# Kernel optimization log

Hardware: AMD Instinct MI355X
Metric: run time of the kernel (lower is better)

Reference implementation:

```python
import jax, jax.numpy as jnp
import numpy as np

N_ITER, N_TAPS, N_DELAY, N_SRC = 2, 4, 1, 4
EPS = 1e-3
TINY = 1e-20
BATCH, N_CHAN, N_FREQ, N_FRAMES = 2, 6, 320, 500


def mag_sq(x):
    return x.real ** 2 + x.imag ** 2


def divide(num, denom, eps):
    return num / jnp.maximum(denom, eps)


def make_xbar(X, n_taps, n_delay):
    # X: (..., c, f, n) -> X_bar: (..., c, f, t, n); tap t is X delayed by n_delay + t
    n = X.shape[-1]
    pad = [(0, 0)] * (X.ndim - 1)
    taps = [jnp.pad(X, pad + [(n_delay + t, 0)])[..., :n] for t in range(n_taps)]
    return jnp.stack(taps, axis=-2)


def background_update(W, H, C_XX, C_XbarX, eps=1e-5):
    # recompute J from W, H and input covariances (ridge-loaded solve)
    n_src = W.shape[-3]
    A1 = jnp.einsum('...sfc,...cfd->...fsd', W, C_XX)
    A2 = jnp.einsum('...sfdt,...dtfc->...fsc', H, C_XbarX)
    Am = A1 + A2
    mat = Am[..., :n_src]
    load = jnp.abs(jnp.diagonal(mat, axis1=-2, axis2=-1)).sum(axis=-1)[..., None, None]
    load = jnp.maximum(load * eps, eps) * jnp.eye(n_src, dtype=mat.dtype)
    load = jax.lax.stop_gradient(load)
    J_H = jnp.linalg.solve(mat + load, Am[..., n_src:])
    return jnp.moveaxis(J_H.conj(), -1, -3)  # (..., n_bak, f, n_src)


def iss_type1(src, Y, w, eps):
    n = Y.shape[-1]
    Ys = Y[..., src, :, :]
    vn = jnp.einsum('...cfn,...cfn,...fn->...cf', w, Y, Ys.conj()) / n
    vd = jnp.einsum('...cfn,...fn->...cf', w, mag_sq(Ys)) / n
    v = divide(vn, vd, eps)
    vs = 1.0 - 1.0 / jnp.sqrt(jnp.maximum(vd[..., src, :], eps))
    return v.at[..., src, :].set(vs.astype(v.dtype))


def iss_type2(Y, Zs, w, eps):
    vn = jnp.einsum('...cfn,...cfn,...fn->...cf', w, Y, Zs.conj())
    vd = jnp.einsum('...cfn,...fn->...cf', w, mag_sq(Zs))
    return divide(vn, vd, eps)


def iss_type3(src, tap, Y, X_bar, w, eps):
    Xst = X_bar[..., src, :, tap, :]
    vn = jnp.einsum('...cfn,...cfn,...fn->...cf', w, Y, Xst.conj())
    vd = jnp.einsum('...cfn,...fn->...cf', w, mag_sq(Xst))
    return divide(vn, vd, eps)


def mat_up1(W, H, A, v, src, eps):
    Wn = W - jnp.einsum('...cf,...fd->...cfd', v, W[..., src, :, :])
    Hn = H - jnp.einsum('...cf,...fdt->...cfdt', v, H[..., src, :, :, :])
    u = jnp.einsum('...sfc,...cf->...sf', A[..., :v.shape[-2]], v)
    u = u / (1.0 - v[..., src:src + 1, :] + eps)
    return Wn, Hn, A.at[..., src].add(u)


def mat_up2(W, J, A, v, g, eps):
    n_src = W.shape[-3]
    v2 = v[..., :n_src, :] + jnp.einsum('...sfc,...cf->...sf', W[..., n_src:], v[..., n_src:, :])
    W1 = W[..., :n_src] - jnp.einsum('...cf,...fd->...cfd', v[..., :n_src, :], g)
    Wn = jnp.concatenate([W1, W[..., n_src:]], axis=-1)
    Jn = J - jnp.einsum('...cf,...fd->...cfd', v[..., n_src:, :], g)
    Av = jnp.einsum('...sfc,...cf->...sf', A[..., :v2.shape[-2]], v2)
    gA = jnp.einsum('...fs,...sfc->...fc', g, A[..., :g.shape[-1], :, :])
    denom = 1.0 - jnp.einsum('...cf,...fc->...f', v2, gA)
    mul = denom.conj() / (mag_sq(denom) + eps)
    An = A + jnp.einsum('...sf,...fc->...sfc', Av, gA * mul[..., None])
    return Wn, Jn, An


def bak_update_vector(p, d, g, eps):
    gdg = jnp.sum(mag_sq(g) / (d + eps), axis=-2)
    gdp = jnp.sum(g.conj() * p / (d + eps), axis=-2)
    b = 1.0 - gdp
    b1 = mag_sq(b)
    a = b1 * gdg + TINY
    beta = (-b1 + jnp.sqrt(b1 ** 2 + 4.0 * a)) / (2.0 * a)
    ell1 = beta * b
    ell2 = (1.0 / jnp.sqrt(eps + gdg)).astype(ell1.dtype)
    ell = jnp.where(b1 > eps ** 2, ell1, ell2)
    return (p - ell[..., None, :] * g) / (d + eps)


def bak_update(bak, Y, Z, X, W, J, A, w, eps):
    n_src, n_freq, n_frames = Y.shape[-3:]
    n_chan = X.shape[-3]
    Zs = Z[..., bak, :, :] + X[..., n_src + bak, :, :]
    norm = 1.0 / n_frames
    ones = jnp.ones(w.shape[:-3] + (n_chan - n_src, n_freq, n_frames), w.dtype)
    wz = jnp.concatenate([w, ones], axis=-3)
    YZ = jnp.concatenate([Y, Z], axis=-3)
    p = jnp.einsum('...cfn,...cfn,...fn->...cf', YZ, wz, Zs.conj()) * norm
    d = jnp.einsum('...cfn,...fn->...cf', wz, mag_sq(Zs)) * norm
    A2 = jnp.concatenate([A, jnp.einsum('...sfc,...cfd->...sfd', A, W[..., n_src:])], axis=-1)
    g = jnp.einsum('...fs,...sfc->...cf', J[..., bak, :, :], A2).conj()
    v = bak_update_vector(p, d, g, eps)
    YZ = YZ - jnp.einsum('...cf,...fn->...cfn', v, Zs)
    return v, YZ[..., :n_src, :, :], YZ[..., n_src:, :, :]


def iss_updates(Y, X, X_bar, W, H, A, w, J, Z, eps):
    n_src = Y.shape[-3]
    n_chan = X.shape[-3]
    n_taps = X_bar.shape[-2]
    n_bak = n_chan - n_src
    # 1) background rows (structured type-2 updates)
    for bak in range(n_bak):
        v, Y, Z = bak_update(bak, Y, Z, X, W, J, A, w, eps)
        g = J[..., bak, :, :]
        W, J, A = mat_up2(W, J, A, v, g, eps)
    # 2) source directions (type 1)
    for src in range(n_src):
        v = iss_type1(src, Y, w, eps)
        Y = Y - jnp.einsum('...cf,...fn->...cfn', v, Y[..., src, :, :])
        W, H, A = mat_up1(W, H, A, v, src, eps)
    # 3) background directions (type 2)
    for bak in range(n_bak):
        v = iss_type2(Y, Z[..., bak, :, :], w, eps)
        Y = Y - jnp.einsum('...cf,...fn->...cfn', v, Z[..., bak, :, :])
        W = W.at[..., :n_src].add(-jnp.einsum('...cf,...fd->...cfd', v, J[..., bak, :, :]))
        W = W.at[..., n_src + bak].add(v)
    if n_bak > 0:
        # keep A consistent: A = inv(W1 + W2 J) per frequency
        Binv = W[..., :n_src] + jnp.einsum('...sfc,...cfd->...sfd', W[..., n_src:], J)
        A = jnp.moveaxis(jnp.linalg.inv(jnp.moveaxis(Binv, -2, -3)), -3, -2)
    # 4) dereverberation taps (type 3)
    for src in range(n_chan):
        for tap in range(n_taps):
            v = iss_type3(src, tap, Y, X_bar, w, eps)
            Y = Y - jnp.einsum('...cf,...fn->...cfn', v, X_bar[..., src, :, tap, :])
            H = H.at[..., src, tap].add(v)
    return Y, Z, W, H, J, A


def _forward(X):
    batch = X.shape[:-3]
    n_chan, n_freq, n_frames = X.shape[-3:]
    n_src = N_SRC
    X_bar = make_xbar(X, N_TAPS, N_DELAY)
    W = jnp.broadcast_to(jnp.eye(n_src, n_chan, dtype=X.dtype)[:, None, :], batch + (n_src, n_freq, n_chan))
    H = jnp.zeros(batch + (n_src, n_freq, n_chan, N_TAPS), X.dtype)
    A = jnp.broadcast_to(jnp.eye(n_src, dtype=X.dtype)[:, None, :], batch + (n_src, n_freq, n_src))
    # initialize background demixing J from input second-order statistics
    C_XX = jnp.einsum('...cfn,...dfn->...cfd', X, X.conj()) / n_frames
    C_XbarX = jnp.einsum('...dftn,...cfn->...dtfc', X_bar, X.conj()) / n_frames
    J = background_update(W, H, C_XX, C_XbarX)
    Y = X[..., :n_src, :, :]
    Z = jnp.einsum('...cfd,...dfn->...cfn', J, X[..., :n_src, :, :]) - X[..., n_src:, :, :]
    for _ in range(N_ITER):
        # Gauss (time-varying) source-model weights, shared across frequencies
        w = 1.0 / jnp.maximum(jnp.mean(mag_sq(Y), axis=-2, keepdims=True), EPS)
        w = jnp.broadcast_to(w, Y.shape)
        Y, Z, W, H, J, A = iss_updates(Y, X, X_bar, W, H, A, w, J, Z, EPS)
    return Y


def setup_inputs():
    key = jax.random.key(0)
    k1, k2 = jax.random.split(key)
    shape = (BATCH, N_CHAN, N_FREQ, N_FRAMES)
    return {"X_real": jax.random.normal(k1, shape, jnp.float32),
            "X_imag": jax.random.normal(k2, shape, jnp.float32)}


def reference(X_real, X_imag):
    X = jax.lax.complex(X_real, X_imag)
    return _forward(X)
```

## Files before the change

kernel.cpp:

```cpp
#include <hip/hip_runtime.h>

#define NFR 500
#define NFQ 320
#define NB  2
#define NC  6
#define NS  4
#define NBK 2
#define NT  4
#define NDLY 1
#define EPSF 1e-3f
#define TINYF 1e-20f

#define NP   512
#define XPAD 8
#define XLEN (XPAD + NP)
#define NCH  8
#define FPC  (NFQ / NCH)

typedef float f2 __attribute__((ext_vector_type(2)));

__device__ __forceinline__ f2 mk2(float r, float i){ f2 t; t.x = r; t.y = i; return t; }
__device__ __forceinline__ f2 cmul(f2 a, f2 b){ return a.xx*b + a.yy*mk2(-b.y, b.x); }
__device__ __forceinline__ f2 cmulc(f2 a, f2 b){ return b.xx*a + b.yy*mk2(a.y, -a.x); }
__device__ __forceinline__ f2 conjc(f2 a){ return mk2(a.x, -a.y); }
__device__ __forceinline__ float cmag2(f2 a){ return a.x*a.x + a.y*a.y; }
__device__ __forceinline__ f2 cinv(f2 a){ float m = a.x*a.x + a.y*a.y; return mk2(a.x/m, -a.y/m); }

#define DPPF(x, ctrl) __int_as_float(__builtin_amdgcn_mov_dpp(__float_as_int(x), (ctrl), 0xF, 0xF, true))
__device__ __forceinline__ float wred64(float x){
  x += DPPF(x, 0x111);
  x += DPPF(x, 0x112);
  x += DPPF(x, 0x114);
  x += DPPF(x, 0x118);
  x += DPPF(x, 0x142);
  x += DPPF(x, 0x143);
  return __int_as_float(__builtin_amdgcn_readlane(__float_as_int(x), 63));
}

__global__ __launch_bounds__(256) void k_init(
  const float* __restrict__ Xr, const float* __restrict__ Xi,
  f2* __restrict__ Yg, f2* __restrict__ Zg,
  f2* __restrict__ Wg, f2* __restrict__ Jg, f2* __restrict__ Ag)
{
  __shared__ f2 sX[NC][NFR];
  __shared__ f2 sC[NS][NC];
  __shared__ f2 sJl[NBK][NS];

  const int bf = blockIdx.x;
  const int b = bf / NFQ, f = bf % NFQ;
  const int tid = threadIdx.x, wv = tid >> 6, lane = tid & 63;

  for (int c = 0; c < NC; ++c) {
    const size_t base = ((size_t)(b*NC + c)*NFQ + f)*NFR;
    for (int n = tid; n < NFR; n += 256)
      sX[c][n] = mk2(Xr[base+n], Xi[base+n]);
  }
  __syncthreads();

  for (int p = wv; p < NS*NC; p += 4) {
    int s = p / NC, d = p % NC;
    f2 ar2 = mk2(0.f,0.f), ai2 = mk2(0.f,0.f);
    for (int n = lane; n < NFR; n += 64) {
      f2 xs = sX[s][n], xd = sX[d][n];
      ar2 += xs * xd;
      ai2 += xs.yx * mk2(xd.x, -xd.y);
    }
    float ar = wred64(ar2.x + ar2.y), ai = wred64(ai2.x + ai2.y);
    if (lane == 0) sC[s][d] = mk2(ar*(1.f/NFR), ai*(1.f/NFR));
  }
  __syncthreads();

  if (tid == 0) {
    f2 M[NS][NC];
    for (int s = 0; s < NS; ++s)
      for (int d = 0; d < NC; ++d) M[s][d] = sC[s][d];
    float dsum = 0.f;
    for (int s = 0; s < NS; ++s) dsum += sqrtf(cmag2(M[s][s]));
    float load = fmaxf(dsum*1e-5f, 1e-5f);
    for (int s = 0; s < NS; ++s) M[s][s].x += load;
    for (int col = 0; col < NS; ++col) {
      int piv = col; float best = cmag2(M[col][col]);
      for (int r = col+1; r < NS; ++r) { float m = cmag2(M[r][col]); if (m > best){best=m; piv=r;} }
      if (piv != col) for (int k = 0; k < NC; ++k) { f2 t=M[col][k]; M[col][k]=M[piv][k]; M[piv][k]=t; }
      f2 ip = cinv(M[col][col]);
      for (int k = col; k < NC; ++k) M[col][k] = cmul(M[col][k], ip);
      for (int r = 0; r < NS; ++r) if (r != col) {
        f2 fac = M[r][col];
        for (int k = col; k < NC; ++k) M[r][k] -= cmul(fac, M[col][k]);
      }
    }
    for (int k = 0; k < NBK; ++k)
      for (int s = 0; s < NS; ++s) sJl[k][s] = conjc(M[s][NS+k]);
  }
  __syncthreads();

  if (tid < NBK*NS) {
    int k = tid / NS, s = tid % NS;
    Jg[((size_t)(b*NBK+k)*NFQ + f)*NS + s] = sJl[k][s];
  } else if (tid < NBK*NS + NS*NC) {
    int t = tid - NBK*NS; int s = t / NC, d = t % NC;
    Wg[((size_t)(b*NS+s)*NFQ + f)*NC + d] = (s==d) ? mk2(1.f,0.f) : mk2(0.f,0.f);
  } else if (tid < NBK*NS + NS*NC + NS*NS) {
    int t = tid - NBK*NS - NS*NC; int s = t / NS, d = t % NS;
    Ag[((size_t)(b*NS+s)*NFQ + f)*NS + d] = (s==d) ? mk2(1.f,0.f) : mk2(0.f,0.f);
  }
  for (int c = 0; c < NS; ++c) {
    const size_t base = ((size_t)(b*NS + c)*NFQ + f)*NFR;
    for (int n = tid; n < NFR; n += 256) Yg[base+n] = sX[c][n];
  }
  for (int k = 0; k < NBK; ++k) {
    const size_t base = ((size_t)(b*NBK + k)*NFQ + f)*NFR;
    for (int n = tid; n < NFR; n += 256) {
      f2 acc = -sX[NS+k][n];
      for (int s = 0; s < NS; ++s) acc += cmul(sJl[k][s], sX[s][n]);
      Zg[base+n] = acc;
    }
  }
}

__global__ __launch_bounds__(512) void k_wpart(const f2* __restrict__ Yg,
                                               float* __restrict__ wacc)
{
  const int bs = blockIdx.x / NCH;
  const int ch = blockIdx.x % NCH;
  const int n  = threadIdx.x;
  if (n >= NFR) return;
  const f2* row = Yg + (size_t)bs*NFQ*NFR;
  f2 acc2 = mk2(0.f,0.f);
  for (int ff = 0; ff < FPC; ++ff) {
    f2 y = row[(size_t)(ch*FPC + ff)*NFR + n];
    acc2 += y*y;
  }
  wacc[((size_t)(ch*NB*NS + bs))*NFR + n] = acc2.x + acc2.y;
}

__global__ __launch_bounds__(256, 4) void k_iter(
  const float* __restrict__ Xr, const float* __restrict__ Xi,
  f2* __restrict__ Yg, f2* __restrict__ Zg,
  f2* __restrict__ Wg, f2* __restrict__ Jg, f2* __restrict__ Ag,
  const float* __restrict__ wacc, float* __restrict__ outR, const int last)
{
  __shared__ f2 sXp[NC][XLEN];
  __shared__ f2 sZ[NBK][NP];
  __shared__ f2 sS[NP];
  __shared__ f2 sW[NS][NC];
  __shared__ f2 sJ[NBK][NS];
  __shared__ f2 sA[NS][NS];
  __shared__ f2 sB[NS][2*NS];
  __shared__ f2 sv[NC], sg[NC], sgo[NS], sp[NC];
  __shared__ float sd[NC];
  __shared__ f2 sAv[NS], sgA[NS], sWsrc[NC];

  const int bf = blockIdx.x;
  const int b = bf / NFQ, f = bf % NFQ;
  const int tid = threadIdx.x, wv = tid >> 6, lane = tid & 63;

  f2 yreg[8];
  float wreg[8];

  for (int c = 0; c < NC; ++c) {
    const size_t base = ((size_t)(b*NC + c)*NFQ + f)*NFR;
    for (int j = tid; j < XLEN; j += 256) {
      int n = j - XPAD;
      sXp[c][j] = (n >= 0 && n < NFR) ? mk2(Xr[base+n], Xi[base+n]) : mk2(0.f,0.f);
    }
  }
  for (int k = 0; k < NBK; ++k) {
    const size_t zb = ((size_t)(b*NBK + k)*NFQ + f)*NFR;
    for (int n = tid; n < NP; n += 256) sZ[k][n] = (n < NFR) ? Zg[zb+n] : mk2(0.f,0.f);
  }
  {
    const size_t yb = ((size_t)(b*NS + wv)*NFQ + f)*NFR;
    const int bs = b*NS + wv;
#pragma unroll
    for (int i = 0; i < 8; ++i) {
      int n = lane + 64*i;
      if (n < NFR) {
        yreg[i] = Yg[yb+n];
        float a = 0.f;
#pragma unroll
        for (int ch = 0; ch < NCH; ++ch) a += wacc[((size_t)(ch*NB*NS + bs))*NFR + n];
        wreg[i] = 1.0f / fmaxf(a * (1.0f/(float)NFQ), EPSF);
      } else { yreg[i] = mk2(0.f,0.f); wreg[i] = 0.f; }
    }
  }
  if (tid < NS*NC) sW[tid/NC][tid%NC] = Wg[((size_t)(b*NS + tid/NC)*NFQ + f)*NC + tid%NC];
  else if (tid < NS*NC + NBK*NS) { int t=tid-NS*NC; sJ[t/NS][t%NS] = Jg[((size_t)(b*NBK+t/NS)*NFQ+f)*NS + t%NS]; }
  else if (tid < NS*NC + NBK*NS + NS*NS) { int t=tid-NS*NC-NBK*NS; sA[t/NS][t%NS] = Ag[((size_t)(b*NS+t/NS)*NFQ+f)*NS + t%NS]; }
  __syncthreads();

  f2 vloc[NC];

  for (int bak = 0; bak < NBK; ++bak) {
    for (int n = tid; n < NP; n += 256)
      sS[n] = sZ[bak][n] + sXp[NS+bak][XPAD+n];
    if (bak > 0 && tid < 16) {
      int s = tid >> 2, c = tid & 3;
      f2 v2[NS];
#pragma unroll
      for (int t = 0; t < NS; ++t)
        v2[t] = vloc[t] + cmul(sW[t][NS+0], vloc[NS+0]) + cmul(sW[t][NS+1], vloc[NS+1]);
      f2 den = mk2(1.f,0.f);
#pragma unroll
      for (int cc = 0; cc < NS; ++cc) den -= cmul(v2[cc], sgA[cc]);
      float m2 = cmag2(den) + EPSF;
      f2 mul = mk2(den.x/m2, -den.y/m2);
      sA[s][c] += cmul(sAv[s], cmul(sgA[c], mul));
    }
    __syncthreads();

    f2 zs[8];
    {
      f2 pr2 = mk2(0.f,0.f), pi2 = mk2(0.f,0.f), dd2 = mk2(0.f,0.f);
#pragma unroll
      for (int i = 0; i < 8; ++i) {
        zs[i] = sS[lane+64*i];
        f2 wy = wreg[i]*yreg[i];
        pr2 += wy * zs[i];
        pi2 += wy.yx * mk2(zs[i].x, -zs[i].y);
        dd2 += (wreg[i]*zs[i]) * zs[i];
      }
      float pr = wred64(pr2.x+pr2.y), pi = wred64(pi2.x+pi2.y), dd = wred64(dd2.x+dd2.y);
      if (lane == 0) { sp[wv] = mk2(pr*(1.f/NFR), pi*(1.f/NFR)); sd[wv] = dd*(1.f/NFR); }
      if (wv < NBK) {
        f2 qr2 = mk2(0.f,0.f), qi2 = mk2(0.f,0.f), qd2 = mk2(0.f,0.f);
#pragma unroll
        for (int i = 0; i < 8; ++i) {
          f2 y = sZ[wv][lane+64*i];
          qr2 += y * zs[i];
          qi2 += y.yx * mk2(zs[i].x, -zs[i].y);
          qd2 += zs[i]*zs[i];
        }
        float qr = wred64(qr2.x+qr2.y), qi = wred64(qi2.x+qi2.y), qd = wred64(qd2.x+qd2.y);
        if (lane == 0) { sp[NS+wv] = mk2(qr*(1.f/NFR), qi*(1.f/NFR)); sd[NS+wv] = qd*(1.f/NFR); }
      }
    }
    if (tid < NC) {
      int c = tid; f2 acc = mk2(0.f,0.f);
      for (int s = 0; s < NS; ++s) {
        f2 a2;
        if (c < NS) a2 = sA[s][c];
        else {
          a2 = mk2(0.f,0.f);
          for (int k = 0; k < NS; ++k) a2 += cmul(sA[s][k], sW[k][c]);
        }
        acc += cmul(sJ[bak][s], a2);
      }
      sg[c] = conjc(acc);
    } else if (tid >= 8 && tid < 8+NS) {
      sgo[tid-8] = sJ[bak][tid-8];
    }
    __syncthreads();

    {
      float gdg = 0.f; f2 gdp = mk2(0.f,0.f);
#pragma unroll
      for (int c = 0; c < NC; ++c) {
        f2 gc = sg[c]; float id = 1.0f/(sd[c] + EPSF);
        gdg += cmag2(gc) * id;
        gdp += id * cmulc(sp[c], gc);
      }
      f2 bb = mk2(1.0f - gdp.x, -gdp.y);
      float b1 = cmag2(bb);
      float a = b1*gdg + TINYF;
      float beta = (-b1 + sqrtf(b1*b1 + 4.0f*a)) / (2.0f*a);
      f2 ell = (b1 > EPSF*EPSF) ? (beta*bb) : mk2(1.0f/sqrtf(EPSF + gdg), 0.f);
#pragma unroll
      for (int c = 0; c < NC; ++c)
        vloc[c] = (1.0f/(sd[c] + EPSF)) * (sp[c] - cmul(ell, sg[c]));
    }
    {
      f2 vc = vloc[wv];
#pragma unroll
      for (int i = 0; i < 8; ++i) yreg[i] -= cmul(vc, zs[i]);
      if (wv < NBK) {
        f2 v2c = vloc[NS+wv];
#pragma unroll
        for (int i = 0; i < 8; ++i) sZ[wv][lane+64*i] -= cmul(v2c, zs[i]);
      }
    }
    __syncthreads();

    if (tid < NS) {
      f2 v2[NS];
#pragma unroll
      for (int t = 0; t < NS; ++t)
        v2[t] = vloc[t] + cmul(sW[t][NS+0], vloc[NS+0]) + cmul(sW[t][NS+1], vloc[NS+1]);
      f2 acc = mk2(0.f,0.f);
#pragma unroll
      for (int c = 0; c < NS; ++c) acc += cmul(sA[tid][c], v2[c]);
      sAv[tid] = acc;
    } else if (tid < 2*NS) {
      int c = tid - NS; f2 acc = mk2(0.f,0.f);
#pragma unroll
      for (int s = 0; s < NS; ++s) acc += cmul(sgo[s], sA[s][c]);
      sgA[c] = acc;
    } else if (tid < 2*NS + 16) {
      int idx = tid - 2*NS; int cc = idx >> 2, d = idx & 3;
      sW[cc][d] -= cmul(vloc[cc], sgo[d]);
    } else if (tid < 2*NS + 16 + 8) {
      int idx = tid - 2*NS - 16; int k = idx >> 2, d = idx & 3;
      sJ[k][d] -= cmul(vloc[NS+k], sgo[d]);
    }
    __syncthreads();
  }

  for (int src = 0; src < NS; ++src) {
    if (wv == src) {
#pragma unroll
      for (int i = 0; i < 8; ++i) sS[lane+64*i] = yreg[i];
    }
    if (tid < NC) sWsrc[tid] = sW[src][tid];
    if (src == 0) {
      if (tid < 16) {
        int s = tid >> 2, c = tid & 3;
        f2 v2[NS];
#pragma unroll
        for (int t = 0; t < NS; ++t)
          v2[t] = vloc[t] + cmul(sW[t][NS+0], vloc[NS+0]) + cmul(sW[t][NS+1], vloc[NS+1]);
        f2 den = mk2(1.f,0.f);
#pragma unroll
        for (int cc = 0; cc < NS; ++cc) den -= cmul(v2[cc], sgA[cc]);
        float m2 = cmag2(den) + EPSF;
        f2 mul = mk2(den.x/m2, -den.y/m2);
        sA[s][c] += cmul(sAv[s], cmul(sgA[c], mul));
      }
    } else if (tid >= 8 && tid < 8+NS) {
      int r = tid - 8, prev = src - 1;
      f2 acc = mk2(0.f,0.f);
#pragma unroll
      for (int c = 0; c < NS; ++c) acc += cmul(sA[r][c], sv[c]);
      float den = 1.0f - sv[prev].x + EPSF;
      sA[r][prev] += (1.0f/den) * acc;
    }
    __syncthreads();

    {
      f2 ys[8];
      f2 nr2 = mk2(0.f,0.f), ni2 = mk2(0.f,0.f), dd2 = mk2(0.f,0.f);
#pragma unroll
      for (int i = 0; i < 8; ++i) {
        ys[i] = sS[lane+64*i];
        f2 wy = wreg[i]*yreg[i];
        nr2 += wy * ys[i];
        ni2 += wy.yx * mk2(ys[i].x, -ys[i].y);
        dd2 += (wreg[i]*ys[i]) * ys[i];
      }
      float nr = wred64(nr2.x+nr2.y)*(1.f/NFR);
      float ni = wred64(ni2.x+ni2.y)*(1.f/NFR);
      float dd = wred64(dd2.x+dd2.y)*(1.f/NFR);
      f2 vc;
      if (wv == src) vc = mk2(1.0f - 1.0f/sqrtf(fmaxf(dd, EPSF)), 0.f);
      else           vc = (1.0f/fmaxf(dd, EPSF)) * mk2(nr, ni);
      if (lane == 0) sv[wv] = vc;
#pragma unroll
      for (int i = 0; i < 8; ++i) yreg[i] -= cmul(vc, ys[i]);
      if (lane < NC) sW[wv][lane] -= cmul(vc, sWsrc[lane]);
    }
    __syncthreads();
  }

  {
    f2 pr0=mk2(0,0), pi0=mk2(0,0), dd0=mk2(0,0);
    f2 pr1=mk2(0,0), pi1=mk2(0,0), dd1=mk2(0,0);
    f2 crr=mk2(0,0), cri=mk2(0,0);
    f2 z0c[8], z1c[8];
#pragma unroll
    for (int i = 0; i < 8; ++i) {
      f2 z0 = sZ[0][lane+64*i], z1 = sZ[1][lane+64*i];
      z0c[i] = z0; z1c[i] = z1;
      f2 wy = wreg[i]*yreg[i];
      f2 wz0 = wreg[i]*z0;
      pr0 += wy * z0;  pi0 += wy.yx * mk2(z0.x, -z0.y);  dd0 += wz0 * z0;
      pr1 += wy * z1;  pi1 += wy.yx * mk2(z1.x, -z1.y);  dd1 += (wreg[i]*z1) * z1;
      crr += wz0 * z1; cri += wz0.yx * mk2(z1.x, -z1.y);
    }
    float P0r = wred64(pr0.x+pr0.y), P0i = wred64(pi0.x+pi0.y), D0 = wred64(dd0.x+dd0.y);
    float P1r = wred64(pr1.x+pr1.y), P1i = wred64(pi1.x+pi1.y), D1 = wred64(dd1.x+dd1.y);
    float Rr  = wred64(crr.x+crr.y), Ri  = wred64(cri.x+cri.y);
    f2 v0 = (1.0f/fmaxf(D0, EPSF)) * mk2(P0r, P0i);
    f2 P1c = mk2(P1r, P1i) - cmul(v0, mk2(Rr, Ri));
    f2 v1 = (1.0f/fmaxf(D1, EPSF)) * P1c;
#pragma unroll
    for (int i = 0; i < 8; ++i) yreg[i] -= cmul(v0, z0c[i]) + cmul(v1, z1c[i]);
    if (lane < NS) sW[wv][lane] -= cmul(v0, sJ[0][lane]) + cmul(v1, sJ[1][lane]);
    else if (lane == NS)   sW[wv][NS+0] += v0;
    else if (lane == NS+1) sW[wv][NS+1] += v1;
  }
  __syncthreads();

  if (tid < 16) {
    int s = tid >> 2, d = tid & 3;
    f2 acc = sW[s][d];
    acc += cmul(sW[s][NS+0], sJ[0][d]);
    acc += cmul(sW[s][NS+1], sJ[1][d]);
    sB[s][d] = acc;
    sB[s][NS+d] = (s==d) ? mk2(1.f,0.f) : mk2(0.f,0.f);
  }
  __syncthreads();
  if (tid == 0) {
    for (int col = 0; col < NS; ++col) {
      int piv = col; float best = cmag2(sB[col][col]);
      for (int r = col+1; r < NS; ++r) { float m = cmag2(sB[r][col]); if (m > best) { best = m; piv = r; } }
      if (piv != col) for (int k = 0; k < 2*NS; ++k) { f2 t = sB[col][k]; sB[col][k] = sB[piv][k]; sB[piv][k] = t; }
      f2 ip = cinv(sB[col][col]);
      for (int k = 0; k < 2*NS; ++k) sB[col][k] = cmul(sB[col][k], ip);
      for (int r = 0; r < NS; ++r) if (r != col) {
        f2 fac = sB[r][col];
        for (int k = 0; k < 2*NS; ++k) sB[r][k] -= cmul(fac, sB[col][k]);
      }
    }
  }

  {
#pragma unroll 1
    for (int src = 0; src < NC; ++src) {
      const f2* __restrict__ xrow = &sXp[src][0];
#pragma unroll
      for (int tap = 0; tap < NT; ++tap) {
        const int xoff = XPAD - (NDLY + tap) + lane;
        f2 xs[8];
        f2 nr2 = mk2(0.f,0.f), ni2 = mk2(0.f,0.f), dd2 = mk2(0.f,0.f);
#pragma unroll
        for (int i = 0; i < 8; ++i) {
          xs[i] = xrow[xoff + 64*i];
          f2 wy = wreg[i]*yreg[i];
          nr2 += wy * xs[i];
          ni2 += wy.yx * mk2(xs[i].x, -xs[i].y);
          dd2 += (wreg[i]*xs[i]) * xs[i];
        }
        float nr = wred64(nr2.x+nr2.y), ni = wred64(ni2.x+ni2.y), dd = wred64(dd2.x+dd2.y);
        f2 vc = (1.0f/fmaxf(dd, EPSF)) * mk2(nr, ni);
#pragma unroll
        for (int i = 0; i < 8; ++i) yreg[i] -= cmul(vc, xs[i]);
      }
    }
  }

  {
    const size_t yb = ((size_t)(b*NS + wv)*NFQ + f)*NFR;
    if (last) {
#pragma unroll
      for (int i = 0; i < 8; ++i) { int n = lane+64*i; if (n < NFR) outR[yb+n] = yreg[i].x; }
    } else {
#pragma unroll
      for (int i = 0; i < 8; ++i) { int n = lane+64*i; if (n < NFR) Yg[yb+n] = yreg[i]; }
    }
  }
  if (!last) {
    __syncthreads();
    for (int k = 0; k < NBK; ++k) {
      const size_t zb = ((size_t)(b*NBK+k)*NFQ + f)*NFR;
      for (int n = tid; n < NFR; n += 256) Zg[zb+n] = sZ[k][n];
    }
    if (tid < NS*NC) Wg[((size_t)(b*NS + tid/NC)*NFQ + f)*NC + tid%NC] = sW[tid/NC][tid%NC];
    else if (tid < NS*NC + NBK*NS) { int t = tid - NS*NC; Jg[((size_t)(b*NBK + t/NS)*NFQ + f)*NS + t%NS] = sJ[t/NS][t%NS]; }
    else if (tid < NS*NC + NBK*NS + NS*NS) { int t = tid - NS*NC - NBK*NS; Ag[((size_t)(b*NS + t/NS)*NFQ + f)*NS + t%NS] = sB[t/NS][NS + t%NS]; }
  }
}

extern "C" void kernel_launch(void* const* d_in, const int* in_sizes, int n_in,
                              void* d_out, int out_size, void* d_ws, size_t ws_size,
                              hipStream_t stream)
{
  (void)in_sizes; (void)n_in; (void)out_size; (void)ws_size;
  const float* Xr = (const float*)d_in[0];
  const float* Xi = (const float*)d_in[1];
  float* outR = (float*)d_out;

  char* ws = (char*)d_ws;
  size_t off = 0;
  f2* Yg = (f2*)(ws + off); off += (size_t)NB*NS*NFQ*NFR*sizeof(f2);
  f2* Zg = (f2*)(ws + off); off += (size_t)NB*NBK*NFQ*NFR*sizeof(f2);
  f2* Wg = (f2*)(ws + off); off += (size_t)NB*NS*NFQ*NC*sizeof(f2);
  f2* Jg = (f2*)(ws + off); off += (size_t)NB*NBK*NFQ*NS*sizeof(f2);
  f2* Ag = (f2*)(ws + off); off += (size_t)NB*NS*NFQ*NS*sizeof(f2);
  float* wacc = (float*)(ws + off); off += (size_t)NCH*NB*NS*NFR*sizeof(float);

  k_init<<<NB*NFQ, 256, 0, stream>>>(Xr, Xi, Yg, Zg, Wg, Jg, Ag);
  for (int it = 0; it < 2; ++it) {
    k_wpart<<<NB*NS*NCH, 512, 0, stream>>>(Yg, wacc);
    k_iter<<<NB*NFQ, 256, 0, stream>>>(Xr, Xi, Yg, Zg, Wg, Jg, Ag, wacc, outR, it == 1);
  }
}
```

Before: 136.4 us.

## Split each channel's frame range across two waves with 512-thread blocks

After: 157.8 us. 1.16x slower.

```diff
diff --git a/kernel.cpp b/kernel.cpp
--- a/kernel.cpp
+++ b/kernel.cpp
@@ -16,6 +16,7 @@
 #define XLEN (XPAD + NP)
 #define NCH  8
 #define FPC  (NFQ / NCH)
+#define NI   4
 
 typedef float f2 __attribute__((ext_vector_type(2)));
 
@@ -134,7 +135,7 @@
   wacc[((size_t)(ch*NB*NS + bs))*NFR + n] = acc2.x + acc2.y;
 }
 
-__global__ __launch_bounds__(256, 4) void k_iter(
+__global__ __launch_bounds__(512, 4) void k_iter(
   const float* __restrict__ Xr, const float* __restrict__ Xi,
   f2* __restrict__ Yg, f2* __restrict__ Zg,
   f2* __restrict__ Wg, f2* __restrict__ Jg, f2* __restrict__ Ag,
@@ -147,39 +148,42 @@
   __shared__ f2 sJ[NBK][NS];
   __shared__ f2 sA[NS][NS];
   __shared__ f2 sB[NS][2*NS];
-  __shared__ f2 sv[NC], sg[NC], sgo[NS], sp[NC];
-  __shared__ float sd[NC];
+  __shared__ f2 sv[NS], sg[NC], sgo[NS];
   __shared__ f2 sAv[NS], sgA[NS], sWsrc[NC];
+  __shared__ float sRed[2][8][8];
 
   const int bf = blockIdx.x;
   const int b = bf / NFQ, f = bf % NFQ;
   const int tid = threadIdx.x, wv = tid >> 6, lane = tid & 63;
-
-  f2 yreg[8];
-  float wreg[8];
+  const int ch = wv & 3;
+  const int h  = wv >> 2;
+  const int fb = h * 256;
+
+  f2 yreg[NI]; float wreg[NI];
 
   for (int c = 0; c < NC; ++c) {
     const size_t base = ((size_t)(b*NC + c)*NFQ + f)*NFR;
-    for (int j = tid; j < XLEN; j += 256) {
+    for (int j = tid; j < XLEN; j += 512) {
       int n = j - XPAD;
       sXp[c][j] = (n >= 0 && n < NFR) ? mk2(Xr[base+n], Xi[base+n]) : mk2(0.f,0.f);
     }
   }
   for (int k = 0; k < NBK; ++k) {
     const size_t zb = ((size_t)(b*NBK + k)*NFQ + f)*NFR;
-    for (int n = tid; n < NP; n += 256) sZ[k][n] = (n < NFR) ? Zg[zb+n] : mk2(0.f,0.f);
+    int n = tid;
+    sZ[k][n] = (n < NFR) ? Zg[zb+n] : mk2(0.f,0.f);
   }
   {
-    const size_t yb = ((size_t)(b*NS + wv)*NFQ + f)*NFR;
-    const int bs = b*NS + wv;
-#pragma unroll
-    for (int i = 0; i < 8; ++i) {
-      int n = lane + 64*i;
+    const size_t yb = ((size_t)(b*NS + ch)*NFQ + f)*NFR;
+    const int bs = b*NS + ch;
+#pragma unroll
+    for (int i = 0; i < NI; ++i) {
+      int n = fb + lane + 64*i;
       if (n < NFR) {
         yreg[i] = Yg[yb+n];
         float a = 0.f;
 #pragma unroll
-        for (int ch = 0; ch < NCH; ++ch) a += wacc[((size_t)(ch*NB*NS + bs))*NFR + n];
+        for (int cc = 0; cc < NCH; ++cc) a += wacc[((size_t)(cc*NB*NS + bs))*NFR + n];
         wreg[i] = 1.0f / fmaxf(a * (1.0f/(float)NFQ), EPSF);
       } else { yreg[i] = mk2(0.f,0.f); wreg[i] = 0.f; }
     }
@@ -192,8 +196,7 @@
   f2 vloc[NC];
 
   for (int bak = 0; bak < NBK; ++bak) {
-    for (int n = tid; n < NP; n += 256)
-      sS[n] = sZ[bak][n] + sXp[NS+bak][XPAD+n];
+    { int n = tid; sS[n] = sZ[bak][n] + sXp[NS+bak][XPAD+n]; }
     if (bak > 0 && tid < 16) {
       int s = tid >> 2, c = tid & 3;
       f2 v2[NS];
@@ -209,30 +212,30 @@
     }
     __syncthreads();
 
-    f2 zs[8];
+    f2 zs[NI];
     {
       f2 pr2 = mk2(0.f,0.f), pi2 = mk2(0.f,0.f), dd2 = mk2(0.f,0.f);
 #pragma unroll
-      for (int i = 0; i < 8; ++i) {
-        zs[i] = sS[lane+64*i];
+      for (int i = 0; i < NI; ++i) {
+        zs[i] = sS[fb + lane + 64*i];
         f2 wy = wreg[i]*yreg[i];
         pr2 += wy * zs[i];
         pi2 += wy.yx * mk2(zs[i].x, -zs[i].y);
         dd2 += (wreg[i]*zs[i]) * zs[i];
       }
       float pr = wred64(pr2.x+pr2.y), pi = wred64(pi2.x+pi2.y), dd = wred64(dd2.x+dd2.y);
-      if (lane == 0) { sp[wv] = mk2(pr*(1.f/NFR), pi*(1.f/NFR)); sd[wv] = dd*(1.f/NFR); }
-      if (wv < NBK) {
+      if (lane == 0) { sRed[0][wv][0]=pr; sRed[0][wv][1]=pi; sRed[0][wv][2]=dd; }
+      if (ch < NBK) {
         f2 qr2 = mk2(0.f,0.f), qi2 = mk2(0.f,0.f), qd2 = mk2(0.f,0.f);
 #pragma unroll
-        for (int i = 0; i < 8; ++i) {
-          f2 y = sZ[wv][lane+64*i];
+        for (int i = 0; i < NI; ++i) {
+          f2 y = sZ[ch][fb + lane + 64*i];
           qr2 += y * zs[i];
           qi2 += y.yx * mk2(zs[i].x, -zs[i].y);
           qd2 += zs[i]*zs[i];
         }
         float qr = wred64(qr2.x+qr2.y), qi = wred64(qi2.x+qi2.y), qd = wred64(qd2.x+qd2.y);
-        if (lane == 0) { sp[NS+wv] = mk2(qr*(1.f/NFR), qi*(1.f/NFR)); sd[NS+wv] = qd*(1.f/NFR); }
+        if (lane == 0) { sRed[0][wv][3]=qr; sRed[0][wv][4]=qi; sRed[0][wv][5]=qd; }
       }
     }
     if (tid < NC) {
@@ -253,12 +256,25 @@
     __syncthreads();
 
     {
+      f2 p[NC]; float d[NC];
+#pragma unroll
+      for (int c = 0; c < NS; ++c) {
+        p[c] = mk2((sRed[0][c][0]+sRed[0][c+4][0])*(1.f/NFR),
+                   (sRed[0][c][1]+sRed[0][c+4][1])*(1.f/NFR));
+        d[c] = (sRed[0][c][2]+sRed[0][c+4][2])*(1.f/NFR);
+      }
+#pragma unroll
+      for (int k = 0; k < NBK; ++k) {
+        p[NS+k] = mk2((sRed[0][k][3]+sRed[0][k+4][3])*(1.f/NFR),
+                      (sRed[0][k][4]+sRed[0][k+4][4])*(1.f/NFR));
+        d[NS+k] = (sRed[0][k][5]+sRed[0][k+4][5])*(1.f/NFR);
+      }
       float gdg = 0.f; f2 gdp = mk2(0.f,0.f);
 #pragma unroll
       for (int c = 0; c < NC; ++c) {
-        f2 gc = sg[c]; float id = 1.0f/(sd[c] + EPSF);
+        f2 gc = sg[c]; float id = 1.0f/(d[c] + EPSF);
         gdg += cmag2(gc) * id;
-        gdp += id * cmulc(sp[c], gc);
+        gdp += id * cmulc(p[c], gc);
       }
       f2 bb = mk2(1.0f - gdp.x, -gdp.y);
       float b1 = cmag2(bb);
@@ -267,16 +283,16 @@
       f2 ell = (b1 > EPSF*EPSF) ? (beta*bb) : mk2(1.0f/sqrtf(EPSF + gdg), 0.f);
 #pragma unroll
       for (int c = 0; c < NC; ++c)
-        vloc[c] = (1.0f/(sd[c] + EPSF)) * (sp[c] - cmul(ell, sg[c]));
+        vloc[c] = (1.0f/(d[c] + EPSF)) * (p[c] - cmul(ell, sg[c]));
     }
     {
-      f2 vc = vloc[wv];
-#pragma unroll
-      for (int i = 0; i < 8; ++i) yreg[i] -= cmul(vc, zs[i]);
-      if (wv < NBK) {
-        f2 v2c = vloc[NS+wv];
-#pragma unroll
-        for (int i = 0; i < 8; ++i) sZ[wv][lane+64*i] -= cmul(v2c, zs[i]);
+      f2 vc = vloc[ch];
+#pragma unroll
+      for (int i = 0; i < NI; ++i) yreg[i] -= cmul(vc, zs[i]);
+      if (ch < NBK) {
+        f2 v2c = vloc[NS+ch];
+#pragma unroll
+        for (int i = 0; i < NI; ++i) sZ[ch][fb + lane + 64*i] -= cmul(v2c, zs[i]);
       }
     }
     __syncthreads();
@@ -306,68 +322,72 @@
   }
 
   for (int src = 0; src < NS; ++src) {
-    if (wv == src) {
-#pragma unroll
-      for (int i = 0; i < 8; ++i) sS[lane+64*i] = yreg[i];
-    }
-    if (tid < NC) sWsrc[tid] = sW[src][tid];
-    if (src == 0) {
-      if (tid < 16) {
-        int s = tid >> 2, c = tid & 3;
-        f2 v2[NS];
-#pragma unroll
-        for (int t = 0; t < NS; ++t)
-          v2[t] = vloc[t] + cmul(sW[t][NS+0], vloc[NS+0]) + cmul(sW[t][NS+1], vloc[NS+1]);
-        f2 den = mk2(1.f,0.f);
-#pragma unroll
-        for (int cc = 0; cc < NS; ++cc) den -= cmul(v2[cc], sgA[cc]);
-        float m2 = cmag2(den) + EPSF;
-        f2 mul = mk2(den.x/m2, -den.y/m2);
-        sA[s][c] += cmul(sAv[s], cmul(sgA[c], mul));
-      }
-    } else if (tid >= 8 && tid < 8+NS) {
-      int r = tid - 8, prev = src - 1;
-      f2 acc = mk2(0.f,0.f);
-#pragma unroll
-      for (int c = 0; c < NS; ++c) acc += cmul(sA[r][c], sv[c]);
-      float den = 1.0f - sv[prev].x + EPSF;
-      sA[r][prev] += (1.0f/den) * acc;
-    }
-    __syncthreads();
-
+    if (ch == src) {
+#pragma unroll
+      for (int i = 0; i < NI; ++i) sS[fb + lane + 64*i] = yreg[i];
+    }
+    if (src == 0 && tid < 16) {
+      int s = tid >> 2, c = tid & 3;
+      f2 v2[NS];
+#pragma unroll
+      for (int t = 0; t < NS; ++t)
+        v2[t] = vloc[t] + cmul(sW[t][NS+0], vloc[NS+0]) + cmul(sW[t][NS+1], vloc[NS+1]);
+      f2 den = mk2(1.f,0.f);
+#pragma unroll
+      for (int cc = 0; cc < NS; ++cc) den -= cmul(v2[cc], sgA[cc]);
+      float m2 = cmag2(den) + EPSF;
+      f2 mul = mk2(den.x/m2, -den.y/m2);
+      sA[s][c] += cmul(sAv[s], cmul(sgA[c], mul));
+    }
+    __syncthreads();
+
+    f2 ys[NI];
     {
-      f2 ys[8];
       f2 nr2 = mk2(0.f,0.f), ni2 = mk2(0.f,0.f), dd2 = mk2(0.f,0.f);
 #pragma unroll
-      for (int i = 0; i < 8; ++i) {
-        ys[i] = sS[lane+64*i];
+      for (int i = 0; i < NI; ++i) {
+        ys[i] = sS[fb + lane + 64*i];
         f2 wy = wreg[i]*yreg[i];
         nr2 += wy * ys[i];
         ni2 += wy.yx * mk2(ys[i].x, -ys[i].y);
         dd2 += (wreg[i]*ys[i]) * ys[i];
       }
-      float nr = wred64(nr2.x+nr2.y)*(1.f/NFR);
-      float ni = wred64(ni2.x+ni2.y)*(1.f/NFR);
-      float dd = wred64(dd2.x+dd2.y)*(1.f/NFR);
+      float nr = wred64(nr2.x+nr2.y), ni = wred64(ni2.x+ni2.y), dd = wred64(dd2.x+dd2.y);
+      if (lane == 0) { sRed[0][wv][0]=nr; sRed[0][wv][1]=ni; sRed[0][wv][2]=dd; }
+    }
+    if (tid < NC) sWsrc[tid] = sW[src][tid];
+    if (src > 0 && tid >= 8 && tid < 8+NS) {
+      int r = tid - 8, prev = src - 1;
+      f2 acc = mk2(0.f,0.f);
+#pragma unroll
+      for (int c = 0; c < NS; ++c) acc += cmul(sA[r][c], sv[c]);
+      float den = 1.0f - sv[prev].x + EPSF;
+      sA[r][prev] += (1.0f/den) * acc;
+    }
+    __syncthreads();
+
+    {
+      float nrs = (sRed[0][ch][0]+sRed[0][ch+4][0])*(1.f/NFR);
+      float nis = (sRed[0][ch][1]+sRed[0][ch+4][1])*(1.f/NFR);
+      float dds = (sRed[0][ch][2]+sRed[0][ch+4][2])*(1.f/NFR);
       f2 vc;
-      if (wv == src) vc = mk2(1.0f - 1.0f/sqrtf(fmaxf(dd, EPSF)), 0.f);
-      else           vc = (1.0f/fmaxf(dd, EPSF)) * mk2(nr, ni);
-      if (lane == 0) sv[wv] = vc;
-#pragma unroll
-      for (int i = 0; i < 8; ++i) yreg[i] -= cmul(vc, ys[i]);
-      if (lane < NC) sW[wv][lane] -= cmul(vc, sWsrc[lane]);
-    }
-    __syncthreads();
+      if (ch == src) vc = mk2(1.0f - 1.0f/sqrtf(fmaxf(dds, EPSF)), 0.f);
+      else           vc = (1.0f/fmaxf(dds, EPSF)) * mk2(nrs, nis);
+      if (h == 0 && lane == 0) sv[ch] = vc;
+#pragma unroll
+      for (int i = 0; i < NI; ++i) yreg[i] -= cmul(vc, ys[i]);
+      if (h == 0 && lane < NC) sW[ch][lane] -= cmul(vc, sWsrc[lane]);
+    }
   }
 
   {
     f2 pr0=mk2(0,0), pi0=mk2(0,0), dd0=mk2(0,0);
     f2 pr1=mk2(0,0), pi1=mk2(0,0), dd1=mk2(0,0);
     f2 crr=mk2(0,0), cri=mk2(0,0);
-    f2 z0c[8], z1c[8];
-#pragma unroll
-    for (int i = 0; i < 8; ++i) {
-      f2 z0 = sZ[0][lane+64*i], z1 = sZ[1][lane+64*i];
+    f2 z0c[NI], z1c[NI];
+#pragma unroll
+    for (int i = 0; i < NI; ++i) {
+      f2 z0 = sZ[0][fb+lane+64*i], z1 = sZ[1][fb+lane+64*i];
       z0c[i] = z0; z1c[i] = z1;
       f2 wy = wreg[i]*yreg[i];
       f2 wz0 = wreg[i]*z0;
@@ -375,54 +395,45 @@
       pr1 += wy * z1;  pi1 += wy.yx * mk2(z1.x, -z1.y);  dd1 += (wreg[i]*z1) * z1;
       crr += wz0 * z1; cri += wz0.yx * mk2(z1.x, -z1.y);
     }
-    float P0r = wred64(pr0.x+pr0.y), P0i = wred64(pi0.x+pi0.y), D0 = wred64(dd0.x+dd0.y);
-    float P1r = wred64(pr1.x+pr1.y), P1i = wred64(pi1.x+pi1.y), D1 = wred64(dd1.x+dd1.y);
-    float Rr  = wred64(crr.x+crr.y), Ri  = wred64(cri.x+cri.y);
+    float r0 = wred64(pr0.x+pr0.y), i0 = wred64(pi0.x+pi0.y), D0p = wred64(dd0.x+dd0.y);
+    float r1 = wred64(pr1.x+pr1.y), i1 = wred64(pi1.x+pi1.y), D1p = wred64(dd1.x+dd1.y);
+    float Rr = wred64(crr.x+crr.y), Ri = wred64(cri.x+cri.y);
+    if (lane == 0) {
+      sRed[1][wv][0]=r0; sRed[1][wv][1]=i0; sRed[1][wv][2]=D0p;
+      sRed[1][wv][3]=r1; sRed[1][wv][4]=i1; sRed[1][wv][5]=D1p;
+      sRed[1][wv][6]=Rr; sRed[1][wv][7]=Ri;
+    }
+    __syncthreads();
+    float P0r = sRed[1][ch][0]+sRed[1][ch+4][0], P0i = sRed[1][ch][1]+sRed[1][ch+4][1];
+    float D0  = sRed[1][ch][2]+sRed[1][ch+4][2];
+    float P1r = sRed[1][ch][3]+sRed[1][ch+4][3], P1i = sRed[1][ch][4]+sRed[1][ch+4][4];
+    float D1  = sRed[1][ch][5]+sRed[1][ch+4][5];
+    float RR  = sRed[1][ch][6]+sRed[1][ch+4][6], RI = sRed[1][ch][7]+sRed[1][ch+4][7];
     f2 v0 = (1.0f/fmaxf(D0, EPSF)) * mk2(P0r, P0i);
-    f2 P1c = mk2(P1r, P1i) - cmul(v0, mk2(Rr, Ri));
+    f2 P1c = mk2(P1r, P1i) - cmul(v0, mk2(RR, RI));
     f2 v1 = (1.0f/fmaxf(D1, EPSF)) * P1c;
 #pragma unroll
-    for (int i = 0; i < 8; ++i) yreg[i] -= cmul(v0, z0c[i]) + cmul(v1, z1c[i]);
-    if (lane < NS) sW[wv][lane] -= cmul(v0, sJ[0][lane]) + cmul(v1, sJ[1][lane]);
-    else if (lane == NS)   sW[wv][NS+0] += v0;
-    else if (lane == NS+1) sW[wv][NS+1] += v1;
+    for (int i = 0; i < NI; ++i) yreg[i] -= cmul(v0, z0c[i]) + cmul(v1, z1c[i]);
+    if (h == 0) {
+      if (lane < NS) sW[ch][lane] -= cmul(v0, sJ[0][lane]) + cmul(v1, sJ[1][lane]);
+      else if (lane == NS)   sW[ch][NS+0] += v0;
+      else if (lane == NS+1) sW[ch][NS+1] += v1;
+    }
   }
   __syncthreads();
 
-  if (tid < 16) {
-    int s = tid >> 2, d = tid & 3;
-    f2 acc = sW[s][d];
-    acc += cmul(sW[s][NS+0], sJ[0][d]);
-    acc += cmul(sW[s][NS+1], sJ[1][d]);
-    sB[s][d] = acc;
-    sB[s][NS+d] = (s==d) ? mk2(1.f,0.f) : mk2(0.f,0.f);
-  }
-  __syncthreads();
-  if (tid == 0) {
-    for (int col = 0; col < NS; ++col) {
-      int piv = col; float best = cmag2(sB[col][col]);
-      for (int r = col+1; r < NS; ++r) { float m = cmag2(sB[r][col]); if (m > best) { best = m; piv = r; } }
-      if (piv != col) for (int k = 0; k < 2*NS; ++k) { f2 t = sB[col][k]; sB[col][k] = sB[piv][k]; sB[piv][k] = t; }
-      f2 ip = cinv(sB[col][col]);
-      for (int k = 0; k < 2*NS; ++k) sB[col][k] = cmul(sB[col][k], ip);
-      for (int r = 0; r < NS; ++r) if (r != col) {
-        f2 fac = sB[r][col];
-        for (int k = 0; k < 2*NS; ++k) sB[r][k] -= cmul(fac, sB[col][k]);
-      }
-    }
-  }
-
   {
+    int par = 0;
 #pragma unroll 1
     for (int src = 0; src < NC; ++src) {
       const f2* __restrict__ xrow = &sXp[src][0];
 #pragma unroll
       for (int tap = 0; tap < NT; ++tap) {
-        const int xoff = XPAD - (NDLY + tap) + lane;
-        f2 xs[8];
+        const int xoff = XPAD - (NDLY + tap) + fb + lane;
+        f2 xs[NI];
         f2 nr2 = mk2(0.f,0.f), ni2 = mk2(0.f,0.f), dd2 = mk2(0.f,0.f);
 #pragma unroll
-        for (int i = 0; i < 8; ++i) {
+        for (int i = 0; i < NI; ++i) {
           xs[i] = xrow[xoff + 64*i];
           f2 wy = wreg[i]*yreg[i];
           nr2 += wy * xs[i];
@@ -430,32 +441,64 @@
           dd2 += (wreg[i]*xs[i]) * xs[i];
         }
         float nr = wred64(nr2.x+nr2.y), ni = wred64(ni2.x+ni2.y), dd = wred64(dd2.x+dd2.y);
-        f2 vc = (1.0f/fmaxf(dd, EPSF)) * mk2(nr, ni);
-#pragma unroll
-        for (int i = 0; i < 8; ++i) yreg[i] -= cmul(vc, xs[i]);
+        if (lane == 0) { sRed[par][wv][0]=nr; sRed[par][wv][1]=ni; sRed[par][wv][2]=dd; }
+        __syncthreads();
+        float nrs = sRed[par][ch][0]+sRed[par][ch+4][0];
+        float nis = sRed[par][ch][1]+sRed[par][ch+4][1];
+        float dds = sRed[par][ch][2]+sRed[par][ch+4][2];
+        f2 vc = (1.0f/fmaxf(dds, EPSF)) * mk2(nrs, nis);
+#pragma unroll
+        for (int i = 0; i < NI; ++i) yreg[i] -= cmul(vc, xs[i]);
+        par ^= 1;
       }
     }
   }
 
   {
-    const size_t yb = ((size_t)(b*NS + wv)*NFQ + f)*NFR;
+    const size_t yb = ((size_t)(b*NS + ch)*NFQ + f)*NFR;
     if (last) {
 #pragma unroll
-      for (int i = 0; i < 8; ++i) { int n = lane+64*i; if (n < NFR) outR[yb+n] = yreg[i].x; }
+      for (int i = 0; i < NI; ++i) { int n = fb+lane+64*i; if (n < NFR) outR[yb+n] = yreg[i].x; }
     } else {
 #pragma unroll
-      for (int i = 0; i < 8; ++i) { int n = lane+64*i; if (n < NFR) Yg[yb+n] = yreg[i]; }
-    }
-  }
-  if (!last) {
-    __syncthreads();
-    for (int k = 0; k < NBK; ++k) {
-      const size_t zb = ((size_t)(b*NBK+k)*NFQ + f)*NFR;
-      for (int n = tid; n < NFR; n += 256) Zg[zb+n] = sZ[k][n];
-    }
-    if (tid < NS*NC) Wg[((size_t)(b*NS + tid/NC)*NFQ + f)*NC + tid%NC] = sW[tid/NC][tid%NC];
-    else if (tid < NS*NC + NBK*NS) { int t = tid - NS*NC; Jg[((size_t)(b*NBK + t/NS)*NFQ + f)*NS + t%NS] = sJ[t/NS][t%NS]; }
-    else if (tid < NS*NC + NBK*NS + NS*NS) { int t = tid - NS*NC - NBK*NS; Ag[((size_t)(b*NS + t/NS)*NFQ + f)*NS + t%NS] = sB[t/NS][NS + t%NS]; }
+      for (int i = 0; i < NI; ++i) { int n = fb+lane+64*i; if (n < NFR) Yg[yb+n] = yreg[i]; }
+      if (tid < 16) {
+        int s = tid >> 2, d = tid & 3;
+        f2 acc = sW[s][d];
+        acc += cmul(sW[s][NS+0], sJ[0][d]);
+        acc += cmul(sW[s][NS+1], sJ[1][d]);
+        sB[s][d] = acc;
+        sB[s][NS+d] = (s==d) ? mk2(1.f,0.f) : mk2(0.f,0.f);
+      }
+      __syncthreads();
+      if (tid == 0) {
+        for (int col = 0; col < NS; ++col) {
+          int piv = col; float best = cmag2(sB[col][col]);
+          for (int r = col+1; r < NS; ++r) { float m = cmag2(sB[r][col]); if (m > best) { best = m; piv = r; } }
+          if (piv != col) for (int k = 0; k < 2*NS; ++k) { f2 t = sB[col][k]; sB[col][k] = sB[piv][k]; sB[piv][k] = t; }
+          f2 ip = cinv(sB[col][col]);
+          for (int k = 0; k < 2*NS; ++k) sB[col][k] = cmul(sB[col][k], ip);
+          for (int r = 0; r < NS; ++r) if (r != col) {
+            f2 fac = sB[r][col];
+            for (int k = 0; k < 2*NS; ++k) sB[r][k] -= cmul(fac, sB[col][k]);
+          }
+        }
+      }
+      for (int k = 0; k < NBK; ++k) {
+        const size_t zb = ((size_t)(b*NBK+k)*NFQ + f)*NFR;
+        int n = tid;
+        if (n < NFR) Zg[zb+n] = sZ[k][n];
+      }
+      if (tid >= 64 && tid < 64 + NS*NC) {
+        int t = tid - 64;
+        Wg[((size_t)(b*NS + t/NC)*NFQ + f)*NC + t%NC] = sW[t/NC][t%NC];
+      } else if (tid >= 96 && tid < 96 + NBK*NS) {
+        int t = tid - 96;
+        Jg[((size_t)(b*NBK + t/NS)*NFQ + f)*NS + t%NS] = sJ[t/NS][t%NS];
+      }
+      __syncthreads();
+      if (tid < NS*NS) Ag[((size_t)(b*NS + (tid>>2))*NFQ + f)*NS + (tid&3)] = sB[tid>>2][NS + (tid&3)];
+    }
   }
 }
 
@@ -480,6 +523,6 @@
   k_init<<<NB*NFQ, 256, 0, stream>>>(Xr, Xi, Yg, Zg, Wg, Jg, Ag);
   for (int it = 0; it < 2; ++it) {
     k_wpart<<<NB*NS*NCH, 512, 0, stream>>>(Yg, wacc);
-    k_iter<<<NB*NFQ, 256, 0, stream>>>(Xr, Xi, Yg, Zg, Wg, Jg, Ag, wacc, outR, it == 1);
+    k_iter<<<NB*NFQ, 512, 0, stream>>>(Xr, Xi, Yg, Zg, Wg, Jg, Ag, wacc, outR, it == 1);
   }
 }
```
